# Kernel optimization log

Hardware: AMD Instinct MI355X
Metric: run time of the kernel (lower is better)

## Reference

```python
import jax, jax.numpy as jnp
import numpy as np

NEG_INF = -1e30
LRELU_SLOPE = 0.01
KEEP_SCALE = 2.0  # 1/(1-p) with p=0.5


def mixed_act(x, tid):
    # x: [B, H], tid: [H] int type ids
    # 0 relu, 1 tanh, 2 sig, 3 'smin'->Softmax, 4 'smax'->Softmin, 5 gelu, 6 lrelu
    relu = jnp.maximum(x, 0.0)
    tanh = jnp.tanh(x)
    sig = jax.nn.sigmoid(x)
    gelu = jax.nn.gelu(x, approximate=False)
    lrelu = jnp.where(x >= 0, x, LRELU_SLOPE * x)
    # softmax/softmin restricted to the columns of that type (matches x[:, idx] gather)
    smin = jax.nn.softmax(jnp.where(tid == 3, x, NEG_INF), axis=1)
    smax = jax.nn.softmax(jnp.where(tid == 4, -x, NEG_INF), axis=1)
    return jnp.select(
        [tid == 0, tid == 1, tid == 2, tid == 3, tid == 4, tid == 5, tid == 6],
        [relu, tanh, sig, smin, smax, gelu, lrelu],
    )


def setup_inputs() -> dict:
    key = jax.random.key(0)
    ks = jax.random.split(key, 16)
    B, D_IN, H, C = 32768, 784, 1024, 10
    s_in, s_h = 1.0 / np.sqrt(D_IN), 1.0 / np.sqrt(H)
    inp = {
        "x": jax.random.normal(ks[0], (B, D_IN), jnp.float32),
        "W0": jax.random.normal(ks[1], (H, D_IN), jnp.float32) * s_in,
        "b0": jax.random.normal(ks[2], (H,), jnp.float32) * s_in,
        "W1": jax.random.normal(ks[3], (H, H), jnp.float32) * s_h,
        "b1": jax.random.normal(ks[4], (H,), jnp.float32) * s_h,
        "W2": jax.random.normal(ks[5], (H, H), jnp.float32) * s_h,
        "b2": jax.random.normal(ks[6], (H,), jnp.float32) * s_h,
        "W3": jax.random.normal(ks[7], (C, H), jnp.float32) * s_h,
        "b3": jax.random.normal(ks[8], (C,), jnp.float32) * s_h,
        "mask1": jax.random.bernoulli(ks[9], 0.5, (B, H)).astype(jnp.float32),
        "mask2": jax.random.bernoulli(ks[10], 0.5, (B, H)).astype(jnp.float32),
        "mask3": jax.random.bernoulli(ks[11], 0.5, (B, H)).astype(jnp.float32),
        "type_ids": jax.random.randint(ks[12], (3, H), 0, 7, jnp.int32),
    }
    return inp


def reference(x, W0, b0, W1, b1, W2, b2, W3, b3, mask1, mask2, mask3, type_ids):
    h = mixed_act(x @ W0.T + b0, type_ids[0])
    h = mixed_act((h * mask1 * KEEP_SCALE) @ W1.T + b1, type_ids[1])
    h = mixed_act((h * mask2 * KEEP_SCALE) @ W2.T + b2, type_ids[2])
    logits = (h * mask3 * KEEP_SCALE) @ W3.T + b3
    out = jax.nn.log_softmax(logits, axis=1)
    return (out, mask1, mask2, mask3)
```

## Files before the change

### kernel.cpp

```cpp
#include <hip/hip_runtime.h>
#include <hip/hip_bf16.h>
#include <cstdint>
#include <cstddef>

typedef __bf16 bf16_t;
typedef bf16_t bf16x8 __attribute__((ext_vector_type(8)));
typedef bf16_t bf16x4 __attribute__((ext_vector_type(4)));
typedef float f32x4 __attribute__((ext_vector_type(4)));

#define NEG_BIG (-1e30f)

__global__ __launch_bounds__(256) void convert_pad(const float* __restrict__ src,
                                                   bf16_t* __restrict__ dst,
                                                   int incols, int outcols) {
    const int row = blockIdx.x;
    const float* s = src + (size_t)row * incols;
    bf16_t* d = dst + (size_t)row * outcols;
    const int n4 = outcols >> 2;
    for (int c = threadIdx.x; c < n4; c += blockDim.x) {
        const int col = c << 2;
        float4 v;
        if (col < incols) v = *(const float4*)(s + col);
        else              v = make_float4(0.f, 0.f, 0.f, 0.f);
        bf16x4 o;
        o[0] = (bf16_t)v.x; o[1] = (bf16_t)v.y; o[2] = (bf16_t)v.z; o[3] = (bf16_t)v.w;
        *(bf16x4*)(d + col) = o;
    }
}

#define BM 128
#define BN 128
#define BK 64

__global__ __launch_bounds__(256) void gemm_bt(const bf16_t* __restrict__ A,
                                               const bf16_t* __restrict__ W,
                                               const float* __restrict__ bias,
                                               bf16_t* __restrict__ Z,
                                               int K, int N) {
    __shared__ __align__(16) bf16_t As[BM * BK];
    __shared__ __align__(16) bf16_t Bs[BN * BK];
    const int tid  = threadIdx.x;
    const int wid  = tid >> 6;
    const int lane = tid & 63;

    const int bid = (int)blockIdx.x;
    const int cpx = (int)gridDim.x >> 3;
    const int swz = (bid & 7) * cpx + (bid >> 3);
    const int nbn = N >> 7;
    const int n0 = (swz % nbn) * BN;
    const int m0 = (swz / nbn) * BM;

    const int wm = (wid >> 1) * 64;
    const int wn = (wid & 1) * 64;

    f32x4 acc[4][4] = {};

    const int srow = wid * 32 + (lane >> 3);
    const int scol = (((lane & 7) ^ ((lane >> 3) & 7)) * 8);
    const bf16_t* Ab = A + (size_t)(m0 + srow) * K + scol;
    const bf16_t* Wb = W + (size_t)(n0 + srow) * K + scol;
    bf16_t* AsW = As + wid * 2048;
    bf16_t* BsW = Bs + wid * 2048;
    const size_t rstep = (size_t)8 * K;

    for (int k0 = 0; k0 < K; k0 += BK) {
        __syncthreads();
        #pragma unroll
        for (int t = 0; t < 4; ++t)
            __builtin_amdgcn_global_load_lds(
                (const __attribute__((address_space(1))) void*)(Ab + k0 + t * rstep),
                (__attribute__((address_space(3))) void*)(AsW + t * 512), 16, 0, 0);
        #pragma unroll
        for (int t = 0; t < 4; ++t)
            __builtin_amdgcn_global_load_lds(
                (const __attribute__((address_space(1))) void*)(Wb + k0 + t * rstep),
                (__attribute__((address_space(3))) void*)(BsW + t * 512), 16, 0, 0);
        __syncthreads();

        const int arow = wm + (lane & 15);
        const int brow = wn + (lane & 15);
        const int qb   = (lane >> 4) * 16;
        const int rxa  = (arow & 7) << 4;
        const int rxb  = (brow & 7) << 4;
        const char* Ac = (const char*)As;
        const char* Bc = (const char*)Bs;

        #pragma unroll
        for (int kh = 0; kh < 2; ++kh) {
            bf16x8 af[4], bfr[4];
            #pragma unroll
            for (int i = 0; i < 4; ++i)
                af[i] = *(const bf16x8*)(Ac + ((((arow + i * 16) << 7) + qb + kh * 64) ^ rxa));
            #pragma unroll
            for (int j = 0; j < 4; ++j)
                bfr[j] = *(const bf16x8*)(Bc + ((((brow + j * 16) << 7) + qb + kh * 64) ^ rxb));
            #pragma unroll
            for (int i = 0; i < 4; ++i)
                #pragma unroll
                for (int j = 0; j < 4; ++j)
                    acc[i][j] = __builtin_amdgcn_mfma_f32_16x16x32_bf16(af[i], bfr[j], acc[i][j], 0, 0, 0);
        }
    }

    const int cq = lane >> 4;
    const int cl = lane & 15;
    #pragma unroll
    for (int j = 0; j < 4; ++j) {
        const int col = n0 + wn + j * 16 + cl;
        const float bj = bias[col];
        #pragma unroll
        for (int i = 0; i < 4; ++i) {
            const int row = m0 + wm + i * 16 + cq * 4;
            #pragma unroll
            for (int r = 0; r < 4; ++r)
                Z[(size_t)(row + r) * N + col] = (bf16_t)(acc[i][j][r] + bj);
        }
    }
}

__global__ __launch_bounds__(256) void act_kernel(const bf16_t* __restrict__ Z,
                                                  const float* __restrict__ mask,
                                                  const int* __restrict__ tids,
                                                  bf16_t* __restrict__ H,
                                                  float* __restrict__ mask_out) {
    const int wid  = threadIdx.x >> 6;
    const int lane = threadIdx.x & 63;
    const int row  = (int)blockIdx.x * 4 + wid;
    const size_t rb = (size_t)row * 1024;

    float p[16], mk[16];
    uint32_t m3 = 0, m4 = 0;
    float s3 = 0.f, s4 = 0.f;

    #pragma unroll
    for (int q = 0; q < 2; ++q) {
        const int c0 = (q * 64 + lane) * 8;
        const bf16x8 z8 = *(const bf16x8*)(Z + rb + c0);
        const int4   ta = *(const int4*)(tids + c0);
        const int4   tb = *(const int4*)(tids + c0 + 4);
        const float4 ma = *(const float4*)(mask + rb + c0);
        const float4 mb = *(const float4*)(mask + rb + c0 + 4);
        const int   tt8[8] = {ta.x, ta.y, ta.z, ta.w, tb.x, tb.y, tb.z, tb.w};
        const float mm8[8] = {ma.x, ma.y, ma.z, ma.w, mb.x, mb.y, mb.z, mb.w};
        #pragma unroll
        for (int j = 0; j < 8; ++j) {
            const int i = q * 8 + j;
            const float zz = (float)z8[j];
            const int tt = tt8[j];
            mk[i] = mm8[j];
            const float az = fabsf(zz);
            const float arg = (tt == 1) ? -2.f * az
                            : (tt == 2) ? -az
                            : (tt == 3) ? zz
                            : (tt == 4) ? -zz : 0.f;
            const float ee = __expf(arg);
            const float r1pe = __builtin_amdgcn_rcpf(1.f + ee);
            const float tha = (1.f - ee) * r1pe;
            const float tnh = (zz >= 0.f) ? tha : -tha;
            const float sg  = ((zz >= 0.f) ? 1.f : ee) * r1pe;
            const float gel = 0.5f * zz * (1.f + erff(zz * 0.70710678f));
            const float pre = (tt == 0) ? fmaxf(zz, 0.f)
                            : (tt == 1) ? tnh
                            : (tt == 2) ? sg
                            : (tt == 3) ? ee
                            : (tt == 4) ? ee
                            : (tt == 5) ? gel
                            : fmaxf(zz, 0.01f * zz);
            p[i] = pre;
            m3 |= (uint32_t)(tt == 3) << i;
            m4 |= (uint32_t)(tt == 4) << i;
            s3 += (tt == 3) ? ee : 0.f;
            s4 += (tt == 4) ? ee : 0.f;
        }
        *(float4*)(mask_out + rb + c0)     = ma;
        *(float4*)(mask_out + rb + c0 + 4) = mb;
    }
    #pragma unroll
    for (int off = 32; off > 0; off >>= 1) {
        s3 += __shfl_xor(s3, off);
        s4 += __shfl_xor(s4, off);
    }
    const float inv3 = 1.f / s3;
    const float inv4 = 1.f / s4;

    #pragma unroll
    for (int q = 0; q < 2; ++q) {
        const int c0 = (q * 64 + lane) * 8;
        bf16x8 h8;
        #pragma unroll
        for (int j = 0; j < 8; ++j) {
            const int i = q * 8 + j;
            const float sc = ((m3 >> i) & 1) ? inv3 : ((m4 >> i) & 1) ? inv4 : 1.f;
            h8[j] = (bf16_t)(p[i] * sc * mk[i] * 2.0f);
        }
        *(bf16x8*)(H + rb + c0) = h8;
    }
}

__global__ __launch_bounds__(256) void act_final(const bf16_t* __restrict__ Z,
                                                 const float* __restrict__ mask,
                                                 const int* __restrict__ tids,
                                                 const bf16_t* __restrict__ W3b,
                                                 const float* __restrict__ b3,
                                                 float* __restrict__ mask_out,
                                                 float* __restrict__ out) {
    __shared__ __align__(16) bf16_t Ws[10 * 1024];
    #pragma unroll
    for (int i = threadIdx.x * 8; i < 10240; i += 2048)
        *(bf16x8*)(Ws + i) = *(const bf16x8*)(W3b + i);
    __syncthreads();

    const int wid  = threadIdx.x >> 6;
    const int lane = threadIdx.x & 63;
    const int row  = (int)blockIdx.x * 4 + wid;
    const size_t rb = (size_t)row * 1024;

    float p[16], mk[16];
    uint32_t m3 = 0, m4 = 0;
    float s3 = 0.f, s4 = 0.f;

    #pragma unroll
    for (int q = 0; q < 2; ++q) {
        const int c0 = (q * 64 + lane) * 8;
        const bf16x8 z8 = *(const bf16x8*)(Z + rb + c0);
        const int4   ta = *(const int4*)(tids + c0);
        const int4   tb = *(const int4*)(tids + c0 + 4);
        const float4 ma = *(const float4*)(mask + rb + c0);
        const float4 mb = *(const float4*)(mask + rb + c0 + 4);
        const int   tt8[8] = {ta.x, ta.y, ta.z, ta.w, tb.x, tb.y, tb.z, tb.w};
        const float mm8[8] = {ma.x, ma.y, ma.z, ma.w, mb.x, mb.y, mb.z, mb.w};
        #pragma unroll
        for (int j = 0; j < 8; ++j) {
            const int i = q * 8 + j;
            const float zz = (float)z8[j];
            const int tt = tt8[j];
            mk[i] = mm8[j];
            const float az = fabsf(zz);
            const float arg = (tt == 1) ? -2.f * az
                            : (tt == 2) ? -az
                            : (tt == 3) ? zz
                            : (tt == 4) ? -zz : 0.f;
            const float ee = __expf(arg);
            const float r1pe = __builtin_amdgcn_rcpf(1.f + ee);
            const float tha = (1.f - ee) * r1pe;
            const float tnh = (zz >= 0.f) ? tha : -tha;
            const float sg  = ((zz >= 0.f) ? 1.f : ee) * r1pe;
            const float gel = 0.5f * zz * (1.f + erff(zz * 0.70710678f));
            const float pre = (tt == 0) ? fmaxf(zz, 0.f)
                            : (tt == 1) ? tnh
                            : (tt == 2) ? sg
                            : (tt == 3) ? ee
                            : (tt == 4) ? ee
                            : (tt == 5) ? gel
                            : fmaxf(zz, 0.01f * zz);
            p[i] = pre;
            m3 |= (uint32_t)(tt == 3) << i;
            m4 |= (uint32_t)(tt == 4) << i;
            s3 += (tt == 3) ? ee : 0.f;
            s4 += (tt == 4) ? ee : 0.f;
        }
        *(float4*)(mask_out + rb + c0)     = ma;
        *(float4*)(mask_out + rb + c0 + 4) = mb;
    }
    #pragma unroll
    for (int off = 32; off > 0; off >>= 1) {
        s3 += __shfl_xor(s3, off);
        s4 += __shfl_xor(s4, off);
    }
    const float inv3 = 1.f / s3;
    const float inv4 = 1.f / s4;

    float acc[10];
    #pragma unroll
    for (int n = 0; n < 10; ++n) acc[n] = 0.f;

    #pragma unroll
    for (int q = 0; q < 2; ++q) {
        const int c0 = (q * 64 + lane) * 8;
        float h[8];
        #pragma unroll
        for (int j = 0; j < 8; ++j) {
            const int i = q * 8 + j;
            const float sc = ((m3 >> i) & 1) ? inv3 : ((m4 >> i) & 1) ? inv4 : 1.f;
            h[j] = p[i] * sc * mk[i] * 2.0f;
        }
        #pragma unroll
        for (int n = 0; n < 10; ++n) {
            const bf16x8 w8 = *(const bf16x8*)(Ws + n * 1024 + c0);
            float d = 0.f;
            #pragma unroll
            for (int j = 0; j < 8; ++j) d += h[j] * (float)w8[j];
            acc[n] += d;
        }
    }

    #pragma unroll
    for (int n = 0; n < 10; ++n)
        #pragma unroll
        for (int off = 32; off > 0; off >>= 1)
            acc[n] += __shfl_xor(acc[n], off);

    if (lane == 0) {
        float lg[10]; float mx = -1e30f;
        #pragma unroll
        for (int n = 0; n < 10; ++n) { lg[n] = acc[n] + b3[n]; mx = fmaxf(mx, lg[n]); }
        float se = 0.f;
        #pragma unroll
        for (int n = 0; n < 10; ++n) se += __expf(lg[n] - mx);
        const float lse = logf(se) + mx;
        #pragma unroll
        for (int n = 0; n < 10; ++n) out[(size_t)row * 10 + n] = lg[n] - lse;
    }
}

extern "C" void kernel_launch(void* const* d_in, const int* in_sizes, int n_in,
                              void* d_out, int out_size, void* d_ws, size_t ws_size,
                              hipStream_t stream) {
    (void)in_sizes; (void)n_in; (void)out_size; (void)ws_size;
    const float* x     = (const float*)d_in[0];
    const float* W0    = (const float*)d_in[1];
    const float* b0    = (const float*)d_in[2];
    const float* W1    = (const float*)d_in[3];
    const float* b1    = (const float*)d_in[4];
    const float* W2    = (const float*)d_in[5];
    const float* b2    = (const float*)d_in[6];
    const float* W3    = (const float*)d_in[7];
    const float* b3    = (const float*)d_in[8];
    const float* mask1 = (const float*)d_in[9];
    const float* mask2 = (const float*)d_in[10];
    const float* mask3 = (const float*)d_in[11];
    const int*   tids  = (const int*)d_in[12];

    float* out = (float*)d_out;
    float* mo1 = out + 327680;
    float* mo2 = mo1 + 33554432;
    float* mo3 = mo2 + 33554432;

    char* ws = (char*)d_ws;
    bf16_t* xb  = (bf16_t*)ws;  ws += (size_t)32768 * 832 * 2;
    bf16_t* W0b = (bf16_t*)ws;  ws += (size_t)1024 * 832 * 2;
    bf16_t* W1b = (bf16_t*)ws;  ws += (size_t)1024 * 1024 * 2;
    bf16_t* W2b = (bf16_t*)ws;  ws += (size_t)1024 * 1024 * 2;
    bf16_t* W3b = (bf16_t*)ws;  ws += (size_t)16 * 1024 * 2;
    bf16_t* Zb  = (bf16_t*)ws;  ws += (size_t)32768 * 1024 * 2;
    bf16_t* hb  = (bf16_t*)ws;  ws += (size_t)32768 * 1024 * 2;

    convert_pad<<<32768, 256, 0, stream>>>(x,  xb,  784, 832);
    convert_pad<<<1024,  256, 0, stream>>>(W0, W0b, 784, 832);
    convert_pad<<<1024,  256, 0, stream>>>(W1, W1b, 1024, 1024);
    convert_pad<<<1024,  256, 0, stream>>>(W2, W2b, 1024, 1024);
    convert_pad<<<10,    256, 0, stream>>>(W3, W3b, 1024, 1024);

    gemm_bt<<<2048, 256, 0, stream>>>(xb, W0b, b0, Zb, 832, 1024);
    act_kernel<<<8192, 256, 0, stream>>>(Zb, mask1, tids, hb, mo1);
    gemm_bt<<<2048, 256, 0, stream>>>(hb, W1b, b1, Zb, 1024, 1024);
    act_kernel<<<8192, 256, 0, stream>>>(Zb, mask2, tids + 1024, hb, mo2);
    gemm_bt<<<2048, 256, 0, stream>>>(hb, W2b, b2, Zb, 1024, 1024);
    act_final<<<8192, 256, 0, stream>>>(Zb, mask3, tids + 2048, W3b, b3, mo3, out);
}
```

Before: 1.131 ms.

## Double-buffer GEMM LDS tiles with BK=32 and shrink first-layer K padding

```diff
diff --git a/kernel.cpp b/kernel.cpp
--- a/kernel.cpp
+++ b/kernel.cpp
@@ -30,15 +30,15 @@
 
 #define BM 128
 #define BN 128
-#define BK 64
+#define BK 32
 
 __global__ __launch_bounds__(256) void gemm_bt(const bf16_t* __restrict__ A,
                                                const bf16_t* __restrict__ W,
                                                const float* __restrict__ bias,
                                                bf16_t* __restrict__ Z,
                                                int K, int N) {
-    __shared__ __align__(16) bf16_t As[BM * BK];
-    __shared__ __align__(16) bf16_t Bs[BN * BK];
+    __shared__ __align__(16) bf16_t As[2][BM * BK];
+    __shared__ __align__(16) bf16_t Bs[2][BN * BK];
     const int tid  = threadIdx.x;
     const int wid  = tid >> 6;
     const int lane = tid & 63;
@@ -55,52 +55,64 @@
 
     f32x4 acc[4][4] = {};
 
-    const int srow = wid * 32 + (lane >> 3);
-    const int scol = (((lane & 7) ^ ((lane >> 3) & 7)) * 8);
-    const bf16_t* Ab = A + (size_t)(m0 + srow) * K + scol;
-    const bf16_t* Wb = W + (size_t)(n0 + srow) * K + scol;
-    bf16_t* AsW = As + wid * 2048;
-    bf16_t* BsW = Bs + wid * 2048;
-    const size_t rstep = (size_t)8 * K;
-
-    for (int k0 = 0; k0 < K; k0 += BK) {
-        __syncthreads();
-        #pragma unroll
-        for (int t = 0; t < 4; ++t)
-            __builtin_amdgcn_global_load_lds(
-                (const __attribute__((address_space(1))) void*)(Ab + k0 + t * rstep),
-                (__attribute__((address_space(3))) void*)(AsW + t * 512), 16, 0, 0);
-        #pragma unroll
-        for (int t = 0; t < 4; ++t)
-            __builtin_amdgcn_global_load_lds(
-                (const __attribute__((address_space(1))) void*)(Wb + k0 + t * rstep),
-                (__attribute__((address_space(3))) void*)(BsW + t * 512), 16, 0, 0);
-        __syncthreads();
-
-        const int arow = wm + (lane & 15);
-        const int brow = wn + (lane & 15);
-        const int qb   = (lane >> 4) * 16;
-        const int rxa  = (arow & 7) << 4;
-        const int rxb  = (brow & 7) << 4;
-        const char* Ac = (const char*)As;
-        const char* Bc = (const char*)Bs;
-
-        #pragma unroll
-        for (int kh = 0; kh < 2; ++kh) {
-            bf16x8 af[4], bfr[4];
-            #pragma unroll
-            for (int i = 0; i < 4; ++i)
-                af[i] = *(const bf16x8*)(Ac + ((((arow + i * 16) << 7) + qb + kh * 64) ^ rxa));
+    const int srow = wid * 32 + (lane >> 2);
+    const int scol = (((lane & 3) ^ ((lane >> 3) & 3)) << 3);
+    const bf16_t* Ap0 = A + (size_t)(m0 + srow) * K + scol;
+    const bf16_t* Ap1 = Ap0 + (size_t)16 * K;
+    const bf16_t* Wp0 = W + (size_t)(n0 + srow) * K + scol;
+    const bf16_t* Wp1 = Wp0 + (size_t)16 * K;
+
+    const int ldsoff = (wid * 2) * 512;
+
+#define STAGE(b, k0)                                                                        \
+    do {                                                                                    \
+        __builtin_amdgcn_global_load_lds(                                                   \
+            (const __attribute__((address_space(1))) void*)(Ap0 + (k0)),                    \
+            (__attribute__((address_space(3))) void*)(&As[(b)][ldsoff]), 16, 0, 0);         \
+        __builtin_amdgcn_global_load_lds(                                                   \
+            (const __attribute__((address_space(1))) void*)(Ap1 + (k0)),                    \
+            (__attribute__((address_space(3))) void*)(&As[(b)][ldsoff + 512]), 16, 0, 0);   \
+        __builtin_amdgcn_global_load_lds(                                                   \
+            (const __attribute__((address_space(1))) void*)(Wp0 + (k0)),                    \
+            (__attribute__((address_space(3))) void*)(&Bs[(b)][ldsoff]), 16, 0, 0);         \
+        __builtin_amdgcn_global_load_lds(                                                   \
+            (const __attribute__((address_space(1))) void*)(Wp1 + (k0)),                    \
+            (__attribute__((address_space(3))) void*)(&Bs[(b)][ldsoff + 512]), 16, 0, 0);   \
+    } while (0)
+
+    const int nk = K >> 5;
+    STAGE(0, 0);
+    __syncthreads();
+
+    const int arow = wm + (lane & 15);
+    const int brow = wn + (lane & 15);
+    const int s    = lane >> 4;
+    const int ka   = ((s ^ ((arow >> 1) & 3)) << 3);
+    const int kb   = ((s ^ ((brow >> 1) & 3)) << 3);
+
+    int cur = 0;
+    for (int t = 0; t < nk; ++t) {
+        if (t + 1 < nk) STAGE(cur ^ 1, (t + 1) << 5);
+
+        const bf16_t* Ac = &As[cur][0];
+        const bf16_t* Bc = &Bs[cur][0];
+        bf16x8 af[4], bfr[4];
+        #pragma unroll
+        for (int i = 0; i < 4; ++i)
+            af[i] = *(const bf16x8*)(Ac + (arow + i * 16) * BK + ka);
+        #pragma unroll
+        for (int j = 0; j < 4; ++j)
+            bfr[j] = *(const bf16x8*)(Bc + (brow + j * 16) * BK + kb);
+        #pragma unroll
+        for (int i = 0; i < 4; ++i)
             #pragma unroll
             for (int j = 0; j < 4; ++j)
-                bfr[j] = *(const bf16x8*)(Bc + ((((brow + j * 16) << 7) + qb + kh * 64) ^ rxb));
-            #pragma unroll
-            for (int i = 0; i < 4; ++i)
-                #pragma unroll
-                for (int j = 0; j < 4; ++j)
-                    acc[i][j] = __builtin_amdgcn_mfma_f32_16x16x32_bf16(af[i], bfr[j], acc[i][j], 0, 0, 0);
-        }
-    }
+                acc[i][j] = __builtin_amdgcn_mfma_f32_16x16x32_bf16(af[i], bfr[j], acc[i][j], 0, 0, 0);
+
+        __syncthreads();
+        cur ^= 1;
+    }
+#undef STAGE
 
     const int cq = lane >> 4;
     const int cl = lane & 15;
@@ -337,21 +349,21 @@
     float* mo3 = mo2 + 33554432;
 
     char* ws = (char*)d_ws;
-    bf16_t* xb  = (bf16_t*)ws;  ws += (size_t)32768 * 832 * 2;
-    bf16_t* W0b = (bf16_t*)ws;  ws += (size_t)1024 * 832 * 2;
+    bf16_t* xb  = (bf16_t*)ws;  ws += (size_t)32768 * 800 * 2;
+    bf16_t* W0b = (bf16_t*)ws;  ws += (size_t)1024 * 800 * 2;
     bf16_t* W1b = (bf16_t*)ws;  ws += (size_t)1024 * 1024 * 2;
     bf16_t* W2b = (bf16_t*)ws;  ws += (size_t)1024 * 1024 * 2;
     bf16_t* W3b = (bf16_t*)ws;  ws += (size_t)16 * 1024 * 2;
     bf16_t* Zb  = (bf16_t*)ws;  ws += (size_t)32768 * 1024 * 2;
     bf16_t* hb  = (bf16_t*)ws;  ws += (size_t)32768 * 1024 * 2;
 
-    convert_pad<<<32768, 256, 0, stream>>>(x,  xb,  784, 832);
-    convert_pad<<<1024,  256, 0, stream>>>(W0, W0b, 784, 832);
+    convert_pad<<<32768, 256, 0, stream>>>(x,  xb,  784, 800);
+    convert_pad<<<1024,  256, 0, stream>>>(W0, W0b, 784, 800);
     convert_pad<<<1024,  256, 0, stream>>>(W1, W1b, 1024, 1024);
     convert_pad<<<1024,  256, 0, stream>>>(W2, W2b, 1024, 1024);
     convert_pad<<<10,    256, 0, stream>>>(W3, W3b, 1024, 1024);
 
-    gemm_bt<<<2048, 256, 0, stream>>>(xb, W0b, b0, Zb, 832, 1024);
+    gemm_bt<<<2048, 256, 0, stream>>>(xb, W0b, b0, Zb, 800, 1024);
     act_kernel<<<8192, 256, 0, stream>>>(Zb, mask1, tids, hb, mo1);
     gemm_bt<<<2048, 256, 0, stream>>>(hb, W1b, b1, Zb, 1024, 1024);
     act_kernel<<<8192, 256, 0, stream>>>(Zb, mask2, tids + 1024, hb, mo2);
```

Result: no change. 1.118 ms (-1.1%).
